# Performance work log

Hardware: AMD Instinct MI355X
Metric: run time of the kernel (lower is better)

The kernel has to match this reference:

```python
import jax, jax.numpy as jnp
import numpy as np

DIM = 256
HEADS = 8
HEAD_DIM = DIM // HEADS
B = 4
Wd, Hd = 48, 48
N = Wd * Hd  # 2304


def _layernorm(x, g, b, eps=1e-5):
    mu = jnp.mean(x, axis=-1, keepdims=True)
    var = jnp.mean(jnp.square(x - mu), axis=-1, keepdims=True)
    return (x - mu) * jax.lax.rsqrt(var + eps) * g + b


def _build_mask(mask):
    # Binarize: <1 -> 0, >0 -> 1 (identity on {0,1} inputs)
    m = (mask > 0).astype(jnp.float32)
    flat = m.reshape(B, m.shape[1], Hd * Wd)[:, 0, :]  # [B, N]
    # mask[b,i,j] zeroed where (flat[j]==0 & flat[i]==1) | (flat[j]==0 & flat[i]==0)
    col0 = flat[:, None, :] == 0   # varies along j
    row = flat[:, :, None]         # varies along i
    bad = (col0 & (row == 1)) | (col0 & (row == 0))
    return (~bad).astype(jnp.float32)  # [B, N, N]


def setup_inputs() -> dict:
    key = jax.random.key(0)
    ks = jax.random.split(key, 12)
    s = 0.02
    x = jax.random.normal(ks[0], (B, N, DIM), jnp.float32)
    mask = jax.random.randint(ks[1], (B, 1, Wd, Hd), 0, 2).astype(jnp.float32)
    inp = {
        "x": x,
        "mask": mask,
        "ln_g": jnp.ones((DIM,), jnp.float32),
        "ln_b": jnp.zeros((DIM,), jnp.float32),
        "Wq": jax.random.normal(ks[2], (DIM, DIM), jnp.float32) * s,
        "bq": jnp.zeros((DIM,), jnp.float32),
        "Wk": jax.random.normal(ks[3], (DIM, DIM), jnp.float32) * s,
        "bk": jnp.zeros((DIM,), jnp.float32),
        "Wv": jax.random.normal(ks[4], (DIM, DIM), jnp.float32) * s,
        "bv": jnp.zeros((DIM,), jnp.float32),
        "Wp": jax.random.normal(ks[5], (DIM, DIM), jnp.float32) * s,
        "bp": jnp.zeros((DIM,), jnp.float32),
    }
    return inp


def reference(x, mask, ln_g, ln_b, Wq, bq, Wk, bk, Wv, bv, Wp, bp):
    Bx, Nx, C = x.shape
    mask_f = _build_mask(mask)  # [B, N, N]
    xn = _layernorm(x, ln_g, ln_b)
    def heads(Wm, bm):
        return (xn @ Wm + bm).reshape(Bx, Nx, HEADS, HEAD_DIM).transpose(0, 2, 1, 3)
    q = heads(Wq, bq)
    k = heads(Wk, bk)
    v = heads(Wv, bv)
    # NOTE: no 1/sqrt(d) scaling in the original; multiplicative 0/1 mask pre-softmax
    attn = jnp.einsum("bhnd,bhmd->bhnm", q, k) * mask_f[:, None, :, :]
    attn = jax.nn.softmax(attn, axis=-1)
    out = jnp.einsum("bhnm,bhmd->bhnd", attn, v)
    out = out.transpose(0, 2, 1, 3).reshape(Bx, Nx, C)
    return out @ Wp + bp
```

## Files before the change

### kernel.cpp

```cpp
#include <hip/hip_runtime.h>
#include <math.h>

typedef __attribute__((ext_vector_type(8))) short short8;
typedef __attribute__((ext_vector_type(4))) float f32x4;

#if __has_builtin(__builtin_amdgcn_exp2f)
#define EXP2F(x) __builtin_amdgcn_exp2f(x)
#else
#define EXP2F(x) exp2f(x)
#endif

constexpr int B   = 4;
constexpr int N   = 2304;
constexpr int DIM = 256;
constexpr int NH  = 8;
constexpr int DH  = 32;
constexpr int M   = B * N;
constexpr int SLOTS = 2336;
constexpr int CST = SLOTS * DH;
constexpr int XPB = SLOTS * DIM;
constexpr int SPLIT = 3;
constexpr float LOG2E = 1.44269504088896f;

__device__ inline unsigned short f2bf(float f) {
    union { float f; unsigned u; } c; c.f = f;
    unsigned u = c.u;
    u += 0x7fffu + ((u >> 16) & 1u);
    return (unsigned short)(u >> 16);
}
__device__ inline float bf2f(unsigned short h) {
    union { unsigned u; float f; } c; c.u = ((unsigned)h) << 16;
    return c.f;
}
__device__ inline unsigned bits(float f) {
    union { float f; unsigned u; } c; c.f = f; return c.u;
}

__device__ inline size_t fo256(int r, int k) {
    return ((size_t)((r >> 4) * 8 + (k >> 5)) << 9)
         + (size_t)(((((k & 31) >> 3) << 4) + (r & 15)) * 8 + (k & 7));
}
__device__ inline size_t foQK(int n, int d) {
    return ((size_t)(n >> 4) << 9)
         + (size_t)((((d >> 3) << 4) + (n & 15)) * 8 + (d & 7));
}
__device__ inline size_t foKI(int slot, int d) {
    int tile = ((slot >> 5) << 1) + (slot & 1);
    int npos = (slot & 31) >> 1;
    return ((size_t)tile << 9)
         + (size_t)((((d >> 3) << 4) + npos) * 8 + (d & 7));
}
__device__ inline size_t foVTC(int d, int key) {
    return ((size_t)((d >> 4) * (SLOTS / 32) + (key >> 5)) << 9)
         + (size_t)(((((key & 31) >> 3) << 4) + (d & 15)) * 8 + (key & 7));
}

__global__ __launch_bounds__(256) void prep_kernel(
    const float* __restrict__ x, const float* __restrict__ g,
    const float* __restrict__ bta, unsigned short* __restrict__ xh,
    const float* __restrict__ Wq, const float* __restrict__ Wk,
    const float* __restrict__ Wv, const float* __restrict__ Wp,
    unsigned short* __restrict__ Wth, unsigned short* __restrict__ Wtl,
    const float* __restrict__ mask, int* __restrict__ inv,
    int* __restrict__ ncp, float* __restrict__ vm)
{
    __shared__ float tbuf[32][33];
    __shared__ int wsum[4];
    int bx = blockIdx.x;
    int t = threadIdx.x;
    if (bx < 2304) {
        int wave = t >> 6, lane = t & 63;
        int row = bx * 4 + wave;
        float4 v = *(const float4*)&x[(size_t)row * DIM + lane * 4];
        float s = v.x + v.y + v.z + v.w;
        #pragma unroll
        for (int o = 32; o > 0; o >>= 1) s += __shfl_xor(s, o, 64);
        float mu = s * (1.0f / DIM);
        float d0 = v.x - mu, d1 = v.y - mu, d2 = v.z - mu, d3 = v.w - mu;
        float s2 = d0 * d0 + d1 * d1 + d2 * d2 + d3 * d3;
        #pragma unroll
        for (int o = 32; o > 0; o >>= 1) s2 += __shfl_xor(s2, o, 64);
        float r = rsqrtf(s2 * (1.0f / DIM) + 1e-5f);
        float4 gg = *(const float4*)&g[lane * 4];
        float4 bb = *(const float4*)&bta[lane * 4];
        ushort4 hi;
        hi.x = f2bf(d0 * r * gg.x + bb.x);
        hi.y = f2bf(d1 * r * gg.y + bb.y);
        hi.z = f2bf(d2 * r * gg.z + bb.z);
        hi.w = f2bf(d3 * r * gg.w + bb.w);
        *(ushort4*)&xh[fo256(row, lane * 4)] = hi;
    } else if (bx < 2560) {
        int idx = bx - 2304;
        int z = idx >> 6, w = idx & 63;
        const float* W = (z == 0) ? Wq : (z == 1) ? Wk : (z == 2) ? Wv : Wp;
        unsigned short* oh = Wth + (size_t)z * DIM * DIM;
        unsigned short* ol = Wtl + (size_t)z * DIM * DIM;
        int tx = t & 31, ty0 = t >> 5;
        int n0 = (w & 7) * 32, k0 = (w >> 3) * 32;
        for (int ty = ty0; ty < 32; ty += 8)
            tbuf[ty][tx] = W[(size_t)(k0 + ty) * DIM + n0 + tx];
        __syncthreads();
        for (int nn = ty0; nn < 32; nn += 8) {
            float v = tbuf[tx][nn];
            unsigned short hh = f2bf(v);
            size_t o = fo256(n0 + nn, k0 + tx);
            oh[o] = hh;
            ol[o] = f2bf(v - bf2f(hh));
        }
    } else {
        int b = bx - 2560;
        int wave = t >> 6, lane = t & 63;
        vm[b * 256 + t] = 0.f;
        int cnt = 0;
        for (int j = t; j < N; j += 256) cnt += (mask[(size_t)b * N + j] > 0.f);
        #pragma unroll
        for (int o = 32; o > 0; o >>= 1) cnt += __shfl_down(cnt, o, 64);
        if (lane == 0) wsum[wave] = cnt;
        __syncthreads();
        int Nc = wsum[0] + wsum[1] + wsum[2] + wsum[3];
        int Nkp = (Nc + 31) & ~31;
        if (t == 0) { ncp[b * 2] = Nc; ncp[b * 2 + 1] = Nkp; }
        int baseK = 0;
        for (int j0 = 0; j0 < N; j0 += 256) {
            int j = j0 + t;
            bool keep = mask[(size_t)b * N + j] > 0.f;
            unsigned long long bal = __ballot(keep);
            int pos = __popcll(bal & ((1ull << lane) - 1ull));
            int wc  = __popcll(bal);
            __syncthreads();
            if (lane == 0) wsum[wave] = wc;
            __syncthreads();
            int wb = 0;
            for (int w = 0; w < wave; ++w) wb += wsum[w];
            int tot = wsum[0] + wsum[1] + wsum[2] + wsum[3];
            int keptBefore = baseK + wb + pos;
            if (keep) inv[(size_t)b * SLOTS + keptBefore] = j;
            else      inv[(size_t)b * SLOTS + Nkp + (j - keptBefore)] = j;
            baseK += tot;
        }
    }
}

__global__ __launch_bounds__(256) void permute_x(
    const unsigned short* __restrict__ xh,
    const int* __restrict__ inv, const int* __restrict__ ncp,
    unsigned short* __restrict__ xph)
{
    int tid = threadIdx.x;
    int wave = tid >> 6, lane = tid & 63;
    int kq = lane >> 4, r = lane & 15;
    int rtg = blockIdx.x * 4 + wave;
    int b = rtg / (SLOTS / 16), rt = rtg % (SLOTS / 16);
    int y = blockIdx.y;
    unsigned short* dst = xph + (size_t)b * XPB;
    int slot = rt * 16 + r;
    int Nc = ncp[b * 2], Nkp = ncp[b * 2 + 1];
    int mend = Nkp + (N - Nc);
    bool pad = (slot >= Nc && slot < Nkp) || slot >= mend;
    int n = pad ? -1 : inv[(size_t)b * SLOTS + slot];
    #pragma unroll
    for (int kt = 0; kt < 4; ++kt) {
        int k0 = (y * 4 + kt) * 32;
        short8 v = {0, 0, 0, 0, 0, 0, 0, 0};
        if (n >= 0) {
            int gn = b * N + n;
            v = *(const short8*)&xh[(((size_t)(gn >> 4) * 8 + (k0 >> 5)) << 9)
                                    + (kq * 16 + (gn & 15)) * 8];
        }
        *(short8*)&dst[(((size_t)(rt * 8 + (k0 >> 5))) << 9) + lane * 8] = v;
    }
}

__global__ __launch_bounds__(256, 8) void gemm_qkv(
    const unsigned short* __restrict__ xh,
    const unsigned short* __restrict__ xph,
    const unsigned short* __restrict__ Wth,
    const float* __restrict__ bq, const float* __restrict__ bk,
    const float* __restrict__ bv, const int* __restrict__ ncp,
    unsigned short* __restrict__ qb, unsigned short* __restrict__ kc,
    unsigned short* __restrict__ vc)
{
    constexpr size_t WSZ = (size_t)DIM * DIM;
    int z = blockIdx.z, bx = blockIdx.x;
    int tid = threadIdx.x;
    int wave = tid >> 6, lane = tid & 63;
    int quad = lane >> 4, l16 = lane & 15;
    const unsigned short *PA, *PB;
    int arow0, brow0, b;
    if (z == 0) {
        if (bx >= 576) return;
        arow0 = (bx >> 3) * 128 + wave * 32;
        brow0 = (bx & 7) * 32;
        b = ((bx >> 3) * 128) / N;
        PA = xh; PB = Wth;
    } else if (z == 1) {
        b = bx / 152;
        int rr = bx % 152;
        arow0 = (rr >> 3) * 128 + wave * 32;
        brow0 = (rr & 7) * 32;
        if (arow0 >= SLOTS) return;
        if (arow0 >= ncp[b * 2 + 1]) return;
        PA = xph + (size_t)b * XPB;
        PB = Wth + WSZ;
    } else {
        if (bx >= 584) return;
        int nidx = bx % 292;
        b = nidx / 73;
        arow0 = (bx / 292) * 128 + wave * 32;
        brow0 = (nidx % 73) * 32;
        PA = Wth + 2 * WSZ;
        PB = xph + (size_t)b * XPB;
    }
    f32x4 acc[2][2] = {};
    #pragma unroll
    for (int k0 = 0; k0 < DIM; k0 += 32) {
        size_t at = (((size_t)(arow0 >> 4) * 8 + (k0 >> 5)) << 9) + lane * 8;
        size_t bt = (((size_t)(brow0 >> 4) * 8 + (k0 >> 5)) << 9) + lane * 8;
        short8 a0 = *(const short8*)&PA[at];
        short8 a1 = *(const short8*)&PA[at + 4096];
        short8 b0 = *(const short8*)&PB[bt];
        short8 b1 = *(const short8*)&PB[bt + 4096];
        acc[0][0] = __builtin_amdgcn_mfma_f32_16x16x32_bf16(a0, b0, acc[0][0], 0, 0, 0);
        acc[0][1] = __builtin_amdgcn_mfma_f32_16x16x32_bf16(a0, b1, acc[0][1], 0, 0, 0);
        acc[1][0] = __builtin_amdgcn_mfma_f32_16x16x32_bf16(a1, b0, acc[1][0], 0, 0, 0);
        acc[1][1] = __builtin_amdgcn_mfma_f32_16x16x32_bf16(a1, b1, acc[1][1], 0, 0, 0);
    }
    if (z == 0) {
        int nbase = arow0 - b * N;
        #pragma unroll
        for (int j = 0; j < 2; ++j) {
            int c = brow0 + j * 16 + l16;
            int h = c >> 5, d = c & 31;
            float bs = bq[c];
            unsigned short* ob = qb + (size_t)(b * NH + h) * ((size_t)N * DH);
            #pragma unroll
            for (int i = 0; i < 2; ++i)
            #pragma unroll
            for (int r = 0; r < 4; ++r) {
                int n = nbase + i * 16 + quad * 4 + r;
                ob[foQK(n, d)] = f2bf((acc[i][j][r] + bs) * LOG2E);
            }
        }
    } else if (z == 1) {
        #pragma unroll
        for (int j = 0; j < 2; ++j) {
            int c = brow0 + j * 16 + l16;
            int h = c >> 5, d = c & 31;
            float bs = bk[c];
            unsigned short* ob = kc + (size_t)(b * NH + h) * CST;
            #pragma unroll
            for (int i = 0; i < 2; ++i)
            #pragma unroll
            for (int r = 0; r < 4; ++r) {
                int slot = arow0 + i * 16 + quad * 4 + r;
                ob[foKI(slot, d)] = f2bf(acc[i][j][r] + bs);
            }
        }
    } else {
        #pragma unroll
        for (int i = 0; i < 2; ++i)
        #pragma unroll
        for (int r = 0; r < 4; ++r) {
            int m = arow0 + i * 16 + quad * 4 + r;
            int h = m >> 5, d = m & 31;
            float bs = bv[m];
            unsigned short* ob = vc + (size_t)(b * NH + h) * CST;
            #pragma unroll
            for (int j = 0; j < 2; ++j) {
                int key = brow0 + j * 16 + l16;
                ob[foVTC(d, key)] = f2bf(acc[i][j][r] + bs);
            }
        }
    }
}

__global__ __launch_bounds__(256, 4) void attn_kernel(
    const unsigned short* __restrict__ Qb,
    const unsigned short* __restrict__ Kc,
    const unsigned short* __restrict__ Vc,
    const int* __restrict__ ncp,
    unsigned short* __restrict__ po, float* __restrict__ pl,
    float* __restrict__ vm)
{
    __shared__ unsigned short pbuf[8 * 16 * 40];
    int tid  = threadIdx.x;
    int wave = tid >> 6, lane = tid & 63;
    int quad = lane >> 4, l16 = lane & 15;
    int bh = blockIdx.y, b = bh >> 3;
    int sp = blockIdx.z;

    if (sp == SPLIT) {
        if (blockIdx.x >= 8) return;
        int kq = quad;
        int Nc = ncp[b * 2], Nkp = ncp[b * 2 + 1];
        int mend = Nkp + (N - Nc);
        int tbeg = Nkp >> 5, tend = (mend + 31) >> 5;
        int wgid = blockIdx.x * 4 + wave;
        const unsigned short* vcb = Vc + (size_t)bh * CST;
        #pragma unroll
        for (int dt = 0; dt < 2; ++dt) {
            float s = 0.f;
            for (int t = tbeg + wgid; t < tend; t += 32) {
                short8 v = *(const short8*)&vcb[((size_t)(dt * (SLOTS / 32) + t) << 9) + lane * 8];
                int keyb = t * 32 + kq * 8;
                #pragma unroll
                for (int j = 0; j < 8; ++j)
                    s += (keyb + j < mend) ? bf2f((unsigned short)v[j]) : 0.f;
            }
            s += __shfl_xor(s, 16, 64);
            s += __shfl_xor(s, 32, 64);
            if (lane < 16) atomicAdd(&vm[bh * 32 + dt * 16 + l16], s);
        }
        return;
    }

    int q0 = (blockIdx.x * 4 + wave) * 32;
    const unsigned short* Qf = Qb + (size_t)bh * ((size_t)N * DH);
    const unsigned short* Kf = Kc + (size_t)bh * CST;
    const unsigned short* Vf = Vc + (size_t)bh * CST;

    int Nc  = ncp[b * 2];
    int Nkp = ncp[b * 2 + 1];
    int chunks = Nkp >> 5;
    int cbeg = (chunks * sp) / SPLIT;
    int cend = (chunks * (sp + 1)) / SPLIT;
    int kbeg = cbeg << 5, kend = cend << 5;

    short8 qA0 = *(const short8*)&Qf[((size_t)(q0 >> 4) << 9) + lane * 8];
    short8 qA1 = *(const short8*)&Qf[((size_t)((q0 >> 4) + 1) << 9) + lane * 8];

    f32x4 o00 = {0,0,0,0}, o01 = {0,0,0,0}, o10 = {0,0,0,0}, o11 = {0,0,0,0};
    float l0[4] = {0,0,0,0}, l1[4] = {0,0,0,0};

    unsigned short* pb0 = &pbuf[(wave * 2 + 0) * 640];
    unsigned short* pb1 = &pbuf[(wave * 2 + 1) * 640];

    short8 kB0 = *(const short8*)&Kf[((size_t)(kbeg >> 4) << 9) + lane * 8];
    short8 kB1 = *(const short8*)&Kf[((size_t)((kbeg >> 4) + 1) << 9) + lane * 8];
    short8 vB0 = *(const short8*)&Vf[((size_t)(kbeg >> 5) << 9) + lane * 8];
    short8 vB1 = *(const short8*)&Vf[((size_t)((SLOTS / 32) + (kbeg >> 5)) << 9) + lane * 8];

    for (int k0 = kbeg; k0 < kend; k0 += 32) {
        int kn = (k0 + 32 < kend) ? k0 + 32 : kbeg;
        short8 nk0 = *(const short8*)&Kf[((size_t)(kn >> 4) << 9) + lane * 8];
        short8 nk1 = *(const short8*)&Kf[((size_t)((kn >> 4) + 1) << 9) + lane * 8];
        short8 nv0 = *(const short8*)&Vf[((size_t)(kn >> 5) << 9) + lane * 8];
        short8 nv1 = *(const short8*)&Vf[((size_t)((SLOTS / 32) + (kn >> 5)) << 9) + lane * 8];

        int key0 = k0 + 2 * l16;
        bool in0 = key0 < Nc;
        bool in1 = key0 + 1 < Nc;
        f32x4 z = {0,0,0,0};
        f32x4 s00 = __builtin_amdgcn_mfma_f32_16x16x32_bf16(qA0, kB0, z, 0, 0, 0);
        f32x4 s01 = __builtin_amdgcn_mfma_f32_16x16x32_bf16(qA0, kB1, z, 0, 0, 0);
        f32x4 s10 = __builtin_amdgcn_mfma_f32_16x16x32_bf16(qA1, kB0, z, 0, 0, 0);
        f32x4 s11 = __builtin_amdgcn_mfma_f32_16x16x32_bf16(qA1, kB1, z, 0, 0, 0);
        #pragma unroll
        for (int r = 0; r < 4; ++r) {
            int row = quad * 4 + r;
            float p00 = in0 ? EXP2F(s00[r]) : 0.f;
            float p01 = in1 ? EXP2F(s01[r]) : 0.f;
            float p10 = in0 ? EXP2F(s10[r]) : 0.f;
            float p11 = in1 ? EXP2F(s11[r]) : 0.f;
            l0[r] += p00 + p01;
            l1[r] += p10 + p11;
            unsigned pk0 = (bits(p00) >> 16) | (bits(p01) & 0xffff0000u);
            unsigned pk1 = (bits(p10) >> 16) | (bits(p11) & 0xffff0000u);
            *(unsigned*)&pb0[row * 40 + 2 * l16] = pk0;
            *(unsigned*)&pb1[row * 40 + 2 * l16] = pk1;
        }
        short8 pA0 = *(const short8*)&pb0[l16 * 40 + quad * 8];
        short8 pA1 = *(const short8*)&pb1[l16 * 40 + quad * 8];
        o00 = __builtin_amdgcn_mfma_f32_16x16x32_bf16(pA0, vB0, o00, 0, 0, 0);
        o01 = __builtin_amdgcn_mfma_f32_16x16x32_bf16(pA0, vB1, o01, 0, 0, 0);
        o10 = __builtin_amdgcn_mfma_f32_16x16x32_bf16(pA1, vB0, o10, 0, 0, 0);
        o11 = __builtin_amdgcn_mfma_f32_16x16x32_bf16(pA1, vB1, o11, 0, 0, 0);

        kB0 = nk0; kB1 = nk1; vB0 = nv0; vB1 = nv1;
    }
    #pragma unroll
    for (int r = 0; r < 4; ++r) {
        #pragma unroll
        for (int off = 1; off < 16; off <<= 1) {
            l0[r] += __shfl_xor(l0[r], off, 64);
            l1[r] += __shfl_xor(l1[r], off, 64);
        }
    }
    size_t pbase = (size_t)(bh * SPLIT + sp) * N;
    #pragma unroll
    for (int r = 0; r < 4; ++r) {
        int row = quad * 4 + r;
        size_t b0 = (pbase + q0 + row) * DH;
        size_t b1 = (pbase + q0 + 16 + row) * DH;
        po[b0 + l16]      = f2bf(o00[r]);
        po[b0 + 16 + l16] = f2bf(o01[r]);
        po[b1 + l16]      = f2bf(o10[r]);
        po[b1 + 16 + l16] = f2bf(o11[r]);
        if (l16 == 0) {
            pl[pbase + q0 + row]      = l0[r];
            pl[pbase + q0 + 16 + row] = l1[r];
        }
    }
}

__global__ __launch_bounds__(256) void combine_kernel(
    const unsigned short* __restrict__ po, const float* __restrict__ pl,
    const float* __restrict__ vm, const int* __restrict__ ncp,
    unsigned short* __restrict__ ahn_hi)
{
    int idx = blockIdx.x * 256 + threadIdx.x;
    int bhq = idx >> 2;
    int dg  = (idx & 3) * 8;
    int bh = bhq / N, q = bhq - bh * N;
    int b = bh >> 3, h = bh & 7;
    int Nc = ncp[b * 2];
    float l = (float)(N - Nc);
    float acc[8];
    {
        float4 m0 = *(const float4*)&vm[bh * 32 + dg];
        float4 m1 = *(const float4*)&vm[bh * 32 + dg + 4];
        acc[0] = m0.x; acc[1] = m0.y; acc[2] = m0.z; acc[3] = m0.w;
        acc[4] = m1.x; acc[5] = m1.y; acc[6] = m1.z; acc[7] = m1.w;
    }
    #pragma unroll
    for (int sp = 0; sp < SPLIT; ++sp) {
        size_t pb = ((size_t)(bh * SPLIT + sp) * N + q) * DH + dg;
        l += pl[(size_t)(bh * SPLIT + sp) * N + q];
        short8 a = *(const short8*)&po[pb];
        #pragma unroll
        for (int j = 0; j < 8; ++j) acc[j] += bf2f((unsigned short)a[j]);
    }
    float inv = 1.f / l;
    union { unsigned short u[8]; short8 v; } hi;
    #pragma unroll
    for (int j = 0; j < 8; ++j) hi.u[j] = f2bf(acc[j] * inv);
    *(short8*)&ahn_hi[fo256(b * N + q, h * 32 + dg)] = hi.v;
}

__global__ __launch_bounds__(256, 8) void gemm_p(
    const unsigned short* __restrict__ Ahi,
    const unsigned short* __restrict__ Wth, const unsigned short* __restrict__ Wtl,
    const float* __restrict__ bias, float* __restrict__ out)
{
    constexpr size_t WSZ = (size_t)DIM * DIM;
    const unsigned short* Bhi = Wth + 3 * WSZ;
    const unsigned short* Blo = Wtl + 3 * WSZ;
    int tid = threadIdx.x;
    int wave = tid >> 6, lane = tid & 63;
    int quad = lane >> 4, l16 = lane & 15;
    int r0 = blockIdx.y * 128 + wave * 32;
    int c0 = blockIdx.x * 16;
    f32x4 acc0 = {}, acc1 = {};
    #pragma unroll
    for (int k0 = 0; k0 < DIM; k0 += 32) {
        size_t at = (((size_t)(r0 >> 4) * 8 + (k0 >> 5)) << 9) + lane * 8;
        size_t bt = (((size_t)(c0 >> 4) * 8 + (k0 >> 5)) << 9) + lane * 8;
        short8 ah0 = *(const short8*)&Ahi[at];
        short8 ah1 = *(const short8*)&Ahi[at + 4096];
        short8 bh = *(const short8*)&Bhi[bt];
        short8 bl = *(const short8*)&Blo[bt];
        acc0 = __builtin_amdgcn_mfma_f32_16x16x32_bf16(ah0, bh, acc0, 0, 0, 0);
        acc0 = __builtin_amdgcn_mfma_f32_16x16x32_bf16(ah0, bl, acc0, 0, 0, 0);
        acc1 = __builtin_amdgcn_mfma_f32_16x16x32_bf16(ah1, bh, acc1, 0, 0, 0);
        acc1 = __builtin_amdgcn_mfma_f32_16x16x32_bf16(ah1, bl, acc1, 0, 0, 0);
    }
    int c = c0 + l16;
    float bs = bias[c];
    #pragma unroll
    for (int r = 0; r < 4; ++r) {
        int R0 = r0 + quad * 4 + r;
        out[(size_t)R0 * DIM + c] = acc0[r] + bs;
        out[(size_t)(R0 + 16) * DIM + c] = acc1[r] + bs;
    }
}

extern "C" void kernel_launch(void* const* d_in, const int* in_sizes, int n_in,
                              void* d_out, int out_size, void* d_ws, size_t ws_size,
                              hipStream_t stream)
{
    const float* x    = (const float*)d_in[0];
    const float* mask = (const float*)d_in[1];
    const float* ln_g = (const float*)d_in[2];
    const float* ln_b = (const float*)d_in[3];
    const float* Wq   = (const float*)d_in[4];
    const float* bq   = (const float*)d_in[5];
    const float* Wk   = (const float*)d_in[6];
    const float* bk   = (const float*)d_in[7];
    const float* Wv   = (const float*)d_in[8];
    const float* bv   = (const float*)d_in[9];
    const float* Wp   = (const float*)d_in[10];
    const float* bp   = (const float*)d_in[11];
    float* out = (float*)d_out;

    constexpr size_t SZ  = (size_t)M * DIM;
    constexpr size_t CSZ = (size_t)B * NH * CST;
    constexpr size_t XSZ = (size_t)B * XPB;
    constexpr size_t WSZ = (size_t)DIM * DIM;
    unsigned short* p = (unsigned short*)d_ws;
    unsigned short* xh = p;  p += SZ;
    unsigned short* xph = p; p += XSZ;
    unsigned short* qb = p;  p += SZ;
    unsigned short* kc = p;  p += CSZ;
    unsigned short* vc = p;  p += CSZ;
    unsigned short* ah = p;  p += SZ;
    unsigned short* wth = p; p += 4 * WSZ;
    unsigned short* wtl = p; p += 4 * WSZ;
    unsigned short* po = p; p += (size_t)B * NH * SPLIT * N * DH;
    float* pl = (float*)p;
    float* vm = pl + (size_t)B * NH * SPLIT * N;
    int* inv = (int*)(vm + (size_t)B * NH * 32);
    int* ncp = inv + (size_t)B * SLOTS;

    prep_kernel<<<2564, 256, 0, stream>>>(
        x, ln_g, ln_b, xh, Wq, Wk, Wv, Wp, wth, wtl, mask, inv, ncp, vm);

    permute_x<<<dim3((B * (SLOTS / 16)) / 4, 2), 256, 0, stream>>>(
        xh, inv, ncp, xph);

    gemm_qkv<<<dim3(608, 1, 3), 256, 0, stream>>>(
        xh, xph, wth, bq, bk, bv, ncp, qb, kc, vc);

    attn_kernel<<<dim3(N / 128, B * NH, SPLIT + 1), 256, 0, stream>>>(
        qb, kc, vc, ncp, po, pl, vm);

    combine_kernel<<<(B * NH * N * 4) / 256, 256, 0, stream>>>(
        po, pl, vm, ncp, ah);

    gemm_p<<<dim3(DIM / 16, M / 128), 256, 0, stream>>>(
        ah, wth, wtl, bp, out);
}
```

Before: 148.0 us.

## Drop split-K attention, fuse combine into attention, compute masked V sums in GEMM

Removes the three-way key split in the attention kernel and the separate combine kernel, so each wave processes all unmasked keys and writes normalized bf16 output straight into the projection-GEMM layout. The column sum of V over masked-out keys is now accumulated with shuffles and atomics in the V epilogue of the QKV GEMM, and V is stored only for kept keys. Blocks shrink to two waves so there are more blocks. This removes the partial-output round trip and one launch, but each block now runs a longer serial key loop with less key-dimension parallelism.

```diff
diff --git a/kernel.cpp b/kernel.cpp
--- a/kernel.cpp
+++ b/kernel.cpp
@@ -19,7 +19,6 @@
 constexpr int SLOTS = 2336;
 constexpr int CST = SLOTS * DH;
 constexpr int XPB = SLOTS * DIM;
-constexpr int SPLIT = 3;
 constexpr float LOG2E = 1.44269504088896f;
 
 __device__ inline unsigned short f2bf(float f) {
@@ -178,7 +177,7 @@
     const float* __restrict__ bq, const float* __restrict__ bk,
     const float* __restrict__ bv, const int* __restrict__ ncp,
     unsigned short* __restrict__ qb, unsigned short* __restrict__ kc,
-    unsigned short* __restrict__ vc)
+    unsigned short* __restrict__ vc, float* __restrict__ vm)
 {
     constexpr size_t WSZ = (size_t)DIM * DIM;
     int z = blockIdx.z, bx = blockIdx.x;
@@ -257,6 +256,10 @@
             }
         }
     } else {
+        int Nc  = ncp[b * 2];
+        int Nkp = ncp[b * 2 + 1];
+        int mend = Nkp + (N - Nc);
+        bool anymask = (brow0 + 32 > Nkp) && (brow0 < mend);
         #pragma unroll
         for (int i = 0; i < 2; ++i)
         #pragma unroll
@@ -265,66 +268,47 @@
             int h = m >> 5, d = m & 31;
             float bs = bv[m];
             unsigned short* ob = vc + (size_t)(b * NH + h) * CST;
+            float vsum = 0.f;
             #pragma unroll
             for (int j = 0; j < 2; ++j) {
                 int key = brow0 + j * 16 + l16;
-                ob[foVTC(d, key)] = f2bf(acc[i][j][r] + bs);
+                float val = acc[i][j][r] + bs;
+                if (key < Nkp) ob[foVTC(d, key)] = f2bf(val);
+                else if (key < mend) vsum += val;
             }
-        }
-    }
-}
-
-__global__ __launch_bounds__(256, 4) void attn_kernel(
+            if (anymask) {
+                vsum += __shfl_xor(vsum, 1, 64);
+                vsum += __shfl_xor(vsum, 2, 64);
+                vsum += __shfl_xor(vsum, 4, 64);
+                vsum += __shfl_xor(vsum, 8, 64);
+                if (l16 == 0) atomicAdd(&vm[(size_t)(b * NH + h) * 32 + d], vsum);
+            }
+        }
+    }
+}
+
+__global__ __launch_bounds__(128, 4) void attn_kernel(
     const unsigned short* __restrict__ Qb,
     const unsigned short* __restrict__ Kc,
     const unsigned short* __restrict__ Vc,
     const int* __restrict__ ncp,
-    unsigned short* __restrict__ po, float* __restrict__ pl,
-    float* __restrict__ vm)
-{
-    __shared__ unsigned short pbuf[8 * 16 * 40];
+    const float* __restrict__ vm,
+    unsigned short* __restrict__ ah)
+{
+    __shared__ unsigned short pbuf[2 * 2 * 640];
     int tid  = threadIdx.x;
     int wave = tid >> 6, lane = tid & 63;
     int quad = lane >> 4, l16 = lane & 15;
-    int bh = blockIdx.y, b = bh >> 3;
-    int sp = blockIdx.z;
-
-    if (sp == SPLIT) {
-        if (blockIdx.x >= 8) return;
-        int kq = quad;
-        int Nc = ncp[b * 2], Nkp = ncp[b * 2 + 1];
-        int mend = Nkp + (N - Nc);
-        int tbeg = Nkp >> 5, tend = (mend + 31) >> 5;
-        int wgid = blockIdx.x * 4 + wave;
-        const unsigned short* vcb = Vc + (size_t)bh * CST;
-        #pragma unroll
-        for (int dt = 0; dt < 2; ++dt) {
-            float s = 0.f;
-            for (int t = tbeg + wgid; t < tend; t += 32) {
-                short8 v = *(const short8*)&vcb[((size_t)(dt * (SLOTS / 32) + t) << 9) + lane * 8];
-                int keyb = t * 32 + kq * 8;
-                #pragma unroll
-                for (int j = 0; j < 8; ++j)
-                    s += (keyb + j < mend) ? bf2f((unsigned short)v[j]) : 0.f;
-            }
-            s += __shfl_xor(s, 16, 64);
-            s += __shfl_xor(s, 32, 64);
-            if (lane < 16) atomicAdd(&vm[bh * 32 + dt * 16 + l16], s);
-        }
-        return;
-    }
-
-    int q0 = (blockIdx.x * 4 + wave) * 32;
+    int bh = blockIdx.y, b = bh >> 3, h = bh & 7;
+
+    int q0 = (blockIdx.x * 2 + wave) * 32;
     const unsigned short* Qf = Qb + (size_t)bh * ((size_t)N * DH);
     const unsigned short* Kf = Kc + (size_t)bh * CST;
     const unsigned short* Vf = Vc + (size_t)bh * CST;
 
     int Nc  = ncp[b * 2];
     int Nkp = ncp[b * 2 + 1];
-    int chunks = Nkp >> 5;
-    int cbeg = (chunks * sp) / SPLIT;
-    int cend = (chunks * (sp + 1)) / SPLIT;
-    int kbeg = cbeg << 5, kend = cend << 5;
+    int kend = Nkp;
 
     short8 qA0 = *(const short8*)&Qf[((size_t)(q0 >> 4) << 9) + lane * 8];
     short8 qA1 = *(const short8*)&Qf[((size_t)((q0 >> 4) + 1) << 9) + lane * 8];
@@ -335,13 +319,13 @@
     unsigned short* pb0 = &pbuf[(wave * 2 + 0) * 640];
     unsigned short* pb1 = &pbuf[(wave * 2 + 1) * 640];
 
-    short8 kB0 = *(const short8*)&Kf[((size_t)(kbeg >> 4) << 9) + lane * 8];
-    short8 kB1 = *(const short8*)&Kf[((size_t)((kbeg >> 4) + 1) << 9) + lane * 8];
-    short8 vB0 = *(const short8*)&Vf[((size_t)(kbeg >> 5) << 9) + lane * 8];
-    short8 vB1 = *(const short8*)&Vf[((size_t)((SLOTS / 32) + (kbeg >> 5)) << 9) + lane * 8];
-
-    for (int k0 = kbeg; k0 < kend; k0 += 32) {
-        int kn = (k0 + 32 < kend) ? k0 + 32 : kbeg;
+    short8 kB0 = *(const short8*)&Kf[lane * 8];
+    short8 kB1 = *(const short8*)&Kf[512 + lane * 8];
+    short8 vB0 = *(const short8*)&Vf[lane * 8];
+    short8 vB1 = *(const short8*)&Vf[((size_t)(SLOTS / 32) << 9) + lane * 8];
+
+    for (int k0 = 0; k0 < kend; k0 += 32) {
+        int kn = (k0 + 32 < kend) ? k0 + 32 : 0;
         short8 nk0 = *(const short8*)&Kf[((size_t)(kn >> 4) << 9) + lane * 8];
         short8 nk1 = *(const short8*)&Kf[((size_t)((kn >> 4) + 1) << 9) + lane * 8];
         short8 nv0 = *(const short8*)&Vf[((size_t)(kn >> 5) << 9) + lane * 8];
@@ -386,55 +370,21 @@
             l1[r] += __shfl_xor(l1[r], off, 64);
         }
     }
-    size_t pbase = (size_t)(bh * SPLIT + sp) * N;
+    float vm0 = vm[bh * 32 + l16];
+    float vm1 = vm[bh * 32 + 16 + l16];
+    float lext = (float)(N - Nc);
     #pragma unroll
     for (int r = 0; r < 4; ++r) {
         int row = quad * 4 + r;
-        size_t b0 = (pbase + q0 + row) * DH;
-        size_t b1 = (pbase + q0 + 16 + row) * DH;
-        po[b0 + l16]      = f2bf(o00[r]);
-        po[b0 + 16 + l16] = f2bf(o01[r]);
-        po[b1 + l16]      = f2bf(o10[r]);
-        po[b1 + 16 + l16] = f2bf(o11[r]);
-        if (l16 == 0) {
-            pl[pbase + q0 + row]      = l0[r];
-            pl[pbase + q0 + 16 + row] = l1[r];
-        }
-    }
-}
-
-__global__ __launch_bounds__(256) void combine_kernel(
-    const unsigned short* __restrict__ po, const float* __restrict__ pl,
-    const float* __restrict__ vm, const int* __restrict__ ncp,
-    unsigned short* __restrict__ ahn_hi)
-{
-    int idx = blockIdx.x * 256 + threadIdx.x;
-    int bhq = idx >> 2;
-    int dg  = (idx & 3) * 8;
-    int bh = bhq / N, q = bhq - bh * N;
-    int b = bh >> 3, h = bh & 7;
-    int Nc = ncp[b * 2];
-    float l = (float)(N - Nc);
-    float acc[8];
-    {
-        float4 m0 = *(const float4*)&vm[bh * 32 + dg];
-        float4 m1 = *(const float4*)&vm[bh * 32 + dg + 4];
-        acc[0] = m0.x; acc[1] = m0.y; acc[2] = m0.z; acc[3] = m0.w;
-        acc[4] = m1.x; acc[5] = m1.y; acc[6] = m1.z; acc[7] = m1.w;
-    }
-    #pragma unroll
-    for (int sp = 0; sp < SPLIT; ++sp) {
-        size_t pb = ((size_t)(bh * SPLIT + sp) * N + q) * DH + dg;
-        l += pl[(size_t)(bh * SPLIT + sp) * N + q];
-        short8 a = *(const short8*)&po[pb];
-        #pragma unroll
-        for (int j = 0; j < 8; ++j) acc[j] += bf2f((unsigned short)a[j]);
-    }
-    float inv = 1.f / l;
-    union { unsigned short u[8]; short8 v; } hi;
-    #pragma unroll
-    for (int j = 0; j < 8; ++j) hi.u[j] = f2bf(acc[j] * inv);
-    *(short8*)&ahn_hi[fo256(b * N + q, h * 32 + dg)] = hi.v;
+        float ia = 1.f / (l0[r] + lext);
+        float ib = 1.f / (l1[r] + lext);
+        int ra = b * N + q0 + row;
+        int rb = ra + 16;
+        ah[fo256(ra, h * 32 + l16)]      = f2bf((o00[r] + vm0) * ia);
+        ah[fo256(ra, h * 32 + 16 + l16)] = f2bf((o01[r] + vm1) * ia);
+        ah[fo256(rb, h * 32 + l16)]      = f2bf((o10[r] + vm0) * ib);
+        ah[fo256(rb, h * 32 + 16 + l16)] = f2bf((o11[r] + vm1) * ib);
+    }
 }
 
 __global__ __launch_bounds__(256, 8) void gemm_p(
@@ -505,9 +455,7 @@
     unsigned short* ah = p;  p += SZ;
     unsigned short* wth = p; p += 4 * WSZ;
     unsigned short* wtl = p; p += 4 * WSZ;
-    unsigned short* po = p; p += (size_t)B * NH * SPLIT * N * DH;
-    float* pl = (float*)p;
-    float* vm = pl + (size_t)B * NH * SPLIT * N;
+    float* vm = (float*)p;
     int* inv = (int*)(vm + (size_t)B * NH * 32);
     int* ncp = inv + (size_t)B * SLOTS;
 
@@ -518,13 +466,10 @@
         xh, inv, ncp, xph);
 
     gemm_qkv<<<dim3(608, 1, 3), 256, 0, stream>>>(
-        xh, xph, wth, bq, bk, bv, ncp, qb, kc, vc);
-
-    attn_kernel<<<dim3(N / 128, B * NH, SPLIT + 1), 256, 0, stream>>>(
-        qb, kc, vc, ncp, po, pl, vm);
-
-    combine_kernel<<<(B * NH * N * 4) / 256, 256, 0, stream>>>(
-        po, pl, vm, ncp, ah);
+        xh, xph, wth, bq, bk, bv, ncp, qb, kc, vc, vm);
+
+    attn_kernel<<<dim3(N / 64, B * NH), 128, 0, stream>>>(
+        qb, kc, vc, ncp, vm, ah);
 
     gemm_p<<<dim3(DIM / 16, M / 128), 256, 0, stream>>>(
         ah, wth, wtl, bp, out);
```

Result: slower. 152.3 us (+2.8%).
